# Performance work log

Measured on AMD Instinct MI355X. Metric: run time of the kernel, lower is better.

Reference implementation:

```python
import jax, jax.numpy as jnp
import numpy as np

SHAPES = np.array([[92, 92], [46, 46], [23, 23], [12, 12]], dtype=np.int32)
EMB, HID, H, L, P = 256, 256, 8, 4, 4


def setup_inputs() -> dict:
    key = jax.random.key(0)
    ks = jax.random.split(key, 10)
    I = int(SHAPES.prod(-1).sum())  # 11253 total pyramid pixels
    B, N = 2, I                      # dense encoder-style queries
    img = jax.random.normal(ks[0], (B, I, EMB), jnp.float32)
    queries = jax.random.normal(ks[1], (B, N, EMB), jnp.float32)
    reference_points = jax.random.uniform(ks[2], (B, N, 2), jnp.float32)
    s = 0.02  # keep offsets small so sampling points stay near [0,1]
    W_img = s * jax.random.normal(ks[3], (EMB, HID), jnp.float32)
    b_img = s * jax.random.normal(ks[4], (HID,), jnp.float32)
    W_q = s * jax.random.normal(ks[5], (EMB, H * L * P * 3), jnp.float32)
    b_q = s * jax.random.normal(ks[6], (H * L * P * 3,), jnp.float32)
    W_out = s * jax.random.normal(ks[7], (HID, EMB), jnp.float32)
    b_out = s * jax.random.normal(ks[8], (EMB,), jnp.float32)
    return dict(img=img, shapes=jnp.asarray(SHAPES), queries=queries,
                reference_points=reference_points, W_img=W_img, b_img=b_img,
                W_q=W_q, b_q=b_q, W_out=W_out, b_out=b_out)


def _msda(img_p, shapes_np, sp, aw):
    # img_p: [B,I,H,Cp], sp: [B,N,H,L,P,2] in [0,1] (x,y), aw: [B,N,H,L,P]
    B, I, Hh, Cp = img_p.shape
    N = sp.shape[1]
    imgT = img_p.transpose(0, 2, 1, 3)       # [B,H,I,Cp]
    awT = aw.transpose(0, 2, 1, 3, 4)        # [B,H,N,L,P]
    out = jnp.zeros((B, Hh, N, Cp), img_p.dtype)
    start = 0
    for l in range(shapes_np.shape[0]):
        h, w = int(shapes_np[l, 0]), int(shapes_np[l, 1])
        lvl = imgT[:, :, start:start + h * w]            # [B,H,h*w,Cp]
        start += h * w
        pts = sp[:, :, :, l].transpose(0, 2, 1, 3, 4)    # [B,H,N,P,2]
        # grid_sample(align_corners=True, border): pix = p*(size-1), clamped
        x = jnp.clip(pts[..., 0] * (w - 1), 0.0, w - 1)
        y = jnp.clip(pts[..., 1] * (h - 1), 0.0, h - 1)
        x0 = jnp.floor(x); y0 = jnp.floor(y)
        wx = x - x0; wy = y - y0
        x0i = x0.astype(jnp.int32); y0i = y0.astype(jnp.int32)
        x1i = jnp.minimum(x0i + 1, w - 1); y1i = jnp.minimum(y0i + 1, h - 1)

        def gat(yi, xi):
            idx = (yi * w + xi).reshape(B, Hh, N * P)
            g = jnp.take_along_axis(lvl, idx[..., None], axis=2)
            return g.reshape(B, Hh, N, P, Cp)

        v = (gat(y0i, x0i) * ((1 - wy) * (1 - wx))[..., None]
             + gat(y0i, x1i) * ((1 - wy) * wx)[..., None]
             + gat(y1i, x0i) * (wy * (1 - wx))[..., None]
             + gat(y1i, x1i) * (wy * wx)[..., None])     # [B,H,N,P,Cp]
        out = out + jnp.einsum('bhnpc,bhnp->bhnc', v, awT[:, :, :, l])
    return out.transpose(0, 2, 1, 3)                      # [B,N,H,Cp]


def reference(img, shapes, queries, reference_points, W_img, b_img, W_q, b_q, W_out, b_out):
    shapes_np = np.asarray(jax.device_get(shapes))
    B, I, C = img.shape
    N = queries.shape[1]
    Cp = HID // H
    img_p = (img @ W_img + b_img).reshape(B, I, H, Cp)
    qp = (queries @ W_q + b_q).reshape(B, N, H, L, P, 3)
    offsets = qp[..., :2]
    aw = jax.nn.softmax(qp[..., 2].reshape(B, N, H, L * P), axis=-1).reshape(B, N, H, L, P)
    sp = reference_points[:, :, None, None, None, :] + offsets  # [B,N,H,L,P,2]
    out = _msda(img_p, shapes_np, sp, aw)                        # [B,N,H,Cp]
    return out.reshape(B, N, HID) @ W_out + b_out
```

## Files before the change

kernel.cpp:

```cpp
#include <hip/hip_runtime.h>
#include <math.h>

#define NB    2
#define NQ    11253
#define NEMB  256
#define NHID  256
#define NH    8
#define NCP   32
#define MROWS (NB * NQ)
#define NGRP  (NB * NQ * NH)

__device__ __constant__ int LVL_H[4]     = {92, 46, 23, 12};
__device__ __constant__ int LVL_W[4]     = {92, 46, 23, 12};
__device__ __constant__ int LVL_START[4] = {0, 8464, 10580, 11109};

typedef float  f32x4  __attribute__((ext_vector_type(4)));
typedef __bf16 bf16x8 __attribute__((ext_vector_type(8)));
typedef short  s16x8  __attribute__((ext_vector_type(8)));

#define BM 128
#define BN 128
#define BK 32
#define LDK 40

__global__ __launch_bounds__(256) void gemm_mfma_split(
    const float* __restrict__ A, const float* __restrict__ B,
    const float* __restrict__ bias, float* __restrict__ C,
    int M, int N, int K)
{
    __shared__ __bf16 Ah[BM * LDK];
    __shared__ __bf16 Al[BM * LDK];
    __shared__ __bf16 Bh[BN * LDK];
    __shared__ __bf16 Bl[BN * LDK];

    const int t    = threadIdx.x;
    const int brow = blockIdx.x * BM;
    const int bcol = blockIdx.y * BN;
    const int wave = t >> 6;
    const int lane = t & 63;
    const int wr   = (wave >> 1) * 64;
    const int wc   = (wave & 1) * 64;
    const int l15  = lane & 15;
    const int l4   = lane >> 4;

    f32x4 acc[4][4] = {};

    const int ar = t >> 1;
    const int ak = (t & 1) * 16;
    const int bc2 = (t & 63) * 2;
    const int bk8 = (t >> 6) * 8;

    for (int k0 = 0; k0 < K; k0 += BK) {
        {
            float va[16];
            const int grow = brow + ar;
            if (grow < M) {
                const float* ap = A + (size_t)grow * K + k0 + ak;
                *(float4*)&va[0]  = *(const float4*)(ap + 0);
                *(float4*)&va[4]  = *(const float4*)(ap + 4);
                *(float4*)&va[8]  = *(const float4*)(ap + 8);
                *(float4*)&va[12] = *(const float4*)(ap + 12);
            } else {
                #pragma unroll
                for (int i = 0; i < 16; ++i) va[i] = 0.f;
            }
            bf16x8 h0, h1, l0, l1;
            #pragma unroll
            for (int i = 0; i < 8; ++i) {
                __bf16 h = (__bf16)va[i];
                h0[i] = h;  l0[i] = (__bf16)(va[i] - (float)h);
            }
            #pragma unroll
            for (int i = 0; i < 8; ++i) {
                __bf16 h = (__bf16)va[8 + i];
                h1[i] = h;  l1[i] = (__bf16)(va[8 + i] - (float)h);
            }
            *(bf16x8*)&Ah[ar * LDK + ak]     = h0;
            *(bf16x8*)&Ah[ar * LDK + ak + 8] = h1;
            *(bf16x8*)&Al[ar * LDK + ak]     = l0;
            *(bf16x8*)&Al[ar * LDK + ak + 8] = l1;
        }
        {
            bf16x8 h0, h1, l0, l1;
            #pragma unroll
            for (int j = 0; j < 8; ++j) {
                float2 v = *(const float2*)(B + (size_t)(k0 + bk8 + j) * N + bcol + bc2);
                __bf16 hx = (__bf16)v.x;
                __bf16 hy = (__bf16)v.y;
                h0[j] = hx;  l0[j] = (__bf16)(v.x - (float)hx);
                h1[j] = hy;  l1[j] = (__bf16)(v.y - (float)hy);
            }
            *(bf16x8*)&Bh[(bc2 + 0) * LDK + bk8] = h0;
            *(bf16x8*)&Bh[(bc2 + 1) * LDK + bk8] = h1;
            *(bf16x8*)&Bl[(bc2 + 0) * LDK + bk8] = l0;
            *(bf16x8*)&Bl[(bc2 + 1) * LDK + bk8] = l1;
        }
        __syncthreads();

        s16x8 a_h[4], a_l[4], b_h[4], b_l[4];
        #pragma unroll
        for (int mi = 0; mi < 4; ++mi) {
            int off = (wr + mi * 16 + l15) * LDK + l4 * 8;
            a_h[mi] = *(s16x8*)&Ah[off];
            a_l[mi] = *(s16x8*)&Al[off];
        }
        #pragma unroll
        for (int ni = 0; ni < 4; ++ni) {
            int off = (wc + ni * 16 + l15) * LDK + l4 * 8;
            b_h[ni] = *(s16x8*)&Bh[off];
            b_l[ni] = *(s16x8*)&Bl[off];
        }
        #pragma unroll
        for (int mi = 0; mi < 4; ++mi)
            #pragma unroll
            for (int ni = 0; ni < 4; ++ni) {
                acc[mi][ni] = __builtin_amdgcn_mfma_f32_16x16x32_bf16(a_h[mi], b_h[ni], acc[mi][ni], 0, 0, 0);
                acc[mi][ni] = __builtin_amdgcn_mfma_f32_16x16x32_bf16(a_h[mi], b_l[ni], acc[mi][ni], 0, 0, 0);
                acc[mi][ni] = __builtin_amdgcn_mfma_f32_16x16x32_bf16(a_l[mi], b_h[ni], acc[mi][ni], 0, 0, 0);
            }
        __syncthreads();
    }

    #pragma unroll
    for (int ni = 0; ni < 4; ++ni) {
        const int col = bcol + wc + ni * 16 + l15;
        const float bv = bias[col];
        #pragma unroll
        for (int mi = 0; mi < 4; ++mi) {
            #pragma unroll
            for (int j = 0; j < 4; ++j) {
                int row = brow + wr + mi * 16 + l4 * 4 + j;
                if (row < M) C[(size_t)row * N + col] = acc[mi][ni][j] + bv;
            }
        }
    }
}

__global__ __launch_bounds__(256) void msda_kernel(
    const float* __restrict__ img_p, const float* __restrict__ qp,
    const float* __restrict__ refp, float* __restrict__ out)
{
    __shared__ int smem[16][32][8];
    const int t  = threadIdx.x;
    const int t3 = t & 7;
    const int g  = t >> 3;
    int gid = blockIdx.x * 32 + g;
    const bool valid = gid < NGRP;
    if (!valid) gid = NGRP - 1;
    const int h  = gid & 7;
    const int bn = gid >> 3;
    const int b  = (bn >= NQ) ? 1 : 0;

    const float* q  = qp + (size_t)bn * 384 + h * 48;
    const float rx = refp[bn * 2 + 0];
    const float ry = refp[bn * 2 + 1];

    const float ox0 = q[t3 * 3 + 0],        oy0 = q[t3 * 3 + 1],        sc0 = q[t3 * 3 + 2];
    const float ox1 = q[(t3 + 8) * 3 + 0],  oy1 = q[(t3 + 8) * 3 + 1],  sc1 = q[(t3 + 8) * 3 + 2];

    float mx = fmaxf(sc0, sc1);
    mx = fmaxf(mx, __shfl_xor(mx, 1, 8));
    mx = fmaxf(mx, __shfl_xor(mx, 2, 8));
    mx = fmaxf(mx, __shfl_xor(mx, 4, 8));
    const float e0 = __expf(sc0 - mx);
    const float e1 = __expf(sc1 - mx);
    float sum = e0 + e1;
    sum += __shfl_xor(sum, 1, 8);
    sum += __shfl_xor(sum, 2, 8);
    sum += __shfl_xor(sum, 4, 8);
    const float inv = 1.0f / sum;

    #pragma unroll
    for (int which = 0; which < 2; ++which) {
        const int   s  = which ? (t3 + 8) : t3;
        const float ox = which ? ox1 : ox0;
        const float oy = which ? oy1 : oy0;
        const float aw = (which ? e1 : e0) * inv;
        const int l  = s >> 2;
        const int hh = LVL_H[l], ww = LVL_W[l], st = LVL_START[l];
        float x = (rx + ox) * (float)(ww - 1);
        float y = (ry + oy) * (float)(hh - 1);
        x = fminf(fmaxf(x, 0.f), (float)(ww - 1));
        y = fminf(fmaxf(y, 0.f), (float)(hh - 1));
        const float x0f = floorf(x), y0f = floorf(y);
        const int   x0 = (int)x0f,  y0 = (int)y0f;
        const float wx = x - x0f,   wy = y - y0f;
        const int dxb = (x0 < ww - 1) ? (NH * NCP * 4) : 0;
        const int dyb = (y0 < hh - 1) ? (ww * NH * NCP * 4) : 0;
        const int o00 = (st + y0 * ww + x0) * (NH * NCP * 4);
        const float u0 = aw * (1.f - wx), u1 = aw * wx;
        int4 pa = make_int4(o00, dxb, dyb, __float_as_int(u0 * (1.f - wy)));
        int4 pb = make_int4(__float_as_int(u1 * (1.f - wy)),
                            __float_as_int(u0 * wy),
                            __float_as_int(u1 * wy), 0);
        *(int4*)&smem[s][g][0] = pa;
        *(int4*)&smem[s][g][4] = pb;
    }
    __syncthreads();

    const char* base = (const char*)img_p
        + (((size_t)b * NQ * (NH * NCP) + h * NCP + t3 * 4) * 4);
    f32x4 acc = {0.f, 0.f, 0.f, 0.f};
    #pragma unroll
    for (int s = 0; s < 16; ++s) {
        const int4 pa = *(int4*)&smem[s][g][0];
        const int4 pb = *(int4*)&smem[s][g][4];
        const int o00 = pa.x;
        const int o01 = o00 + pa.y;
        const int o10 = o00 + pa.z;
        const int o11 = o10 + pa.y;
        const f32x4 v00 = *(const f32x4*)(base + o00);
        const f32x4 v01 = *(const f32x4*)(base + o01);
        const f32x4 v10 = *(const f32x4*)(base + o10);
        const f32x4 v11 = *(const f32x4*)(base + o11);
        acc += v00 * __int_as_float(pa.w);
        acc += v01 * __int_as_float(pb.x);
        acc += v10 * __int_as_float(pb.y);
        acc += v11 * __int_as_float(pb.z);
    }
    if (valid)
        *(f32x4*)(out + (size_t)bn * NHID + h * NCP + t3 * 4) = acc;
}

extern "C" void kernel_launch(void* const* d_in, const int* in_sizes, int n_in,
                              void* d_out, int out_size, void* d_ws, size_t ws_size,
                              hipStream_t stream) {
    const float* img     = (const float*)d_in[0];
    const float* queries = (const float*)d_in[2];
    const float* refp    = (const float*)d_in[3];
    const float* W_img   = (const float*)d_in[4];
    const float* b_img   = (const float*)d_in[5];
    const float* W_q     = (const float*)d_in[6];
    const float* b_q     = (const float*)d_in[7];
    const float* W_out   = (const float*)d_in[8];
    const float* b_out   = (const float*)d_in[9];
    float* out = (float*)d_out;

    float* ws = (float*)d_ws;
    float* img_p    = ws;
    float* qp       = img_p + (size_t)MROWS * NHID;
    float* msda_out = qp + (size_t)MROWS * 384;

    const int gRows = (MROWS + BM - 1) / BM;

    gemm_mfma_split<<<dim3(gRows, NHID / BN), 256, 0, stream>>>(
        img, W_img, b_img, img_p, MROWS, NHID, NEMB);
    gemm_mfma_split<<<dim3(gRows, 384 / BN), 256, 0, stream>>>(
        queries, W_q, b_q, qp, MROWS, 384, NEMB);
    msda_kernel<<<(NGRP + 31) / 32, 256, 0, stream>>>(img_p, qp, refp, msda_out);
    gemm_mfma_split<<<dim3(gRows, NEMB / BN), 256, 0, stream>>>(
        msda_out, W_out, b_out, out, MROWS, NEMB, NHID);
}
```

Before: 239.6 us.

## Pre-split GEMM operands into transposed bf16 hi/lo buffers before the GEMMs

Weights are converted once per call into transposed bf16 hi/lo pairs, so the GEMM B-tile loads become contiguous vector loads with no per-tile float-to-bf16 split. When the workspace is large enough, the img and query activations are also pre-split in separate conversion kernels. The MSDA kernel now writes its output directly as bf16 hi/lo for the final GEMM. This adds extra kernel launches and a full extra pass over the activations, trading redundant in-GEMM conversion work (repeated for every column block) against that added memory traffic.

```diff
diff --git a/kernel.cpp b/kernel.cpp
--- a/kernel.cpp
+++ b/kernel.cpp
@@ -16,15 +16,66 @@
 
 typedef float  f32x4  __attribute__((ext_vector_type(4)));
 typedef __bf16 bf16x8 __attribute__((ext_vector_type(8)));
+typedef __bf16 bf16x4v __attribute__((ext_vector_type(4)));
 typedef short  s16x8  __attribute__((ext_vector_type(8)));
+
+__global__ __launch_bounds__(256) void convert_hilo(
+    const float* __restrict__ src, __bf16* __restrict__ hi,
+    __bf16* __restrict__ lo, int nch)
+{
+    int i = blockIdx.x * 256 + threadIdx.x;
+    const int stride = gridDim.x * 256;
+    for (; i < nch; i += stride) {
+        const float* p = src + (size_t)i * 8;
+        float4 a = *(const float4*)p;
+        float4 b = *(const float4*)(p + 4);
+        float v[8] = {a.x, a.y, a.z, a.w, b.x, b.y, b.z, b.w};
+        bf16x8 h, l;
+        #pragma unroll
+        for (int j = 0; j < 8; ++j) {
+            __bf16 hh = (__bf16)v[j];
+            h[j] = hh; l[j] = (__bf16)(v[j] - (float)hh);
+        }
+        *(bf16x8*)(hi + (size_t)i * 8) = h;
+        *(bf16x8*)(lo + (size_t)i * 8) = l;
+    }
+}
+
+__global__ __launch_bounds__(256) void convert_w_T(
+    const float* __restrict__ W_img, const float* __restrict__ W_q,
+    const float* __restrict__ W_out,
+    __bf16* __restrict__ WiTh, __bf16* __restrict__ WiTl,
+    __bf16* __restrict__ WqTh, __bf16* __restrict__ WqTl,
+    __bf16* __restrict__ WoTh, __bf16* __restrict__ WoTl)
+{
+    int idx = blockIdx.x * 256 + threadIdx.x;
+    const float* W; __bf16 *Th, *Tl; int Nn, r;
+    if (idx < 8192)       { W = W_img; Th = WiTh; Tl = WiTl; Nn = 256; r = idx; }
+    else if (idx < 20480) { W = W_q;   Th = WqTh; Tl = WqTl; Nn = 384; r = idx - 8192; }
+    else                  { W = W_out; Th = WoTh; Tl = WoTl; Nn = 256; r = idx - 20480; }
+    const int n  = r % Nn;
+    const int k0 = (r / Nn) * 8;
+    bf16x8 h, l;
+    #pragma unroll
+    for (int j = 0; j < 8; ++j) {
+        float v = W[(size_t)(k0 + j) * Nn + n];
+        __bf16 hh = (__bf16)v;
+        h[j] = hh; l[j] = (__bf16)(v - (float)hh);
+    }
+    *(bf16x8*)(Th + (size_t)n * 256 + k0) = h;
+    *(bf16x8*)(Tl + (size_t)n * 256 + k0) = l;
+}
 
 #define BM 128
 #define BN 128
 #define BK 32
 #define LDK 40
 
-__global__ __launch_bounds__(256) void gemm_mfma_split(
-    const float* __restrict__ A, const float* __restrict__ B,
+template<bool PREA>
+__global__ __launch_bounds__(256) void gemm_mfma(
+    const float* __restrict__ A32,
+    const __bf16* __restrict__ Ah_g, const __bf16* __restrict__ Al_g,
+    const __bf16* __restrict__ BhT, const __bf16* __restrict__ BlT,
     const float* __restrict__ bias, float* __restrict__ C,
     int M, int N, int K)
 {
@@ -47,15 +98,26 @@
 
     const int ar = t >> 1;
     const int ak = (t & 1) * 16;
-    const int bc2 = (t & 63) * 2;
-    const int bk8 = (t >> 6) * 8;
+    const int grow = brow + ar;
+    const int bcr = t >> 1;
 
     for (int k0 = 0; k0 < K; k0 += BK) {
-        {
+        if constexpr (PREA) {
+            s16x8 h0 = {}, h1 = {}, l0 = {}, l1 = {};
+            if (grow < M) {
+                const __bf16* hp = Ah_g + (size_t)grow * K + k0 + ak;
+                const __bf16* lp = Al_g + (size_t)grow * K + k0 + ak;
+                h0 = *(const s16x8*)hp;  h1 = *(const s16x8*)(hp + 8);
+                l0 = *(const s16x8*)lp;  l1 = *(const s16x8*)(lp + 8);
+            }
+            *(s16x8*)&Ah[ar * LDK + ak]     = h0;
+            *(s16x8*)&Ah[ar * LDK + ak + 8] = h1;
+            *(s16x8*)&Al[ar * LDK + ak]     = l0;
+            *(s16x8*)&Al[ar * LDK + ak + 8] = l1;
+        } else {
             float va[16];
-            const int grow = brow + ar;
             if (grow < M) {
-                const float* ap = A + (size_t)grow * K + k0 + ak;
+                const float* ap = A32 + (size_t)grow * K + k0 + ak;
                 *(float4*)&va[0]  = *(const float4*)(ap + 0);
                 *(float4*)&va[4]  = *(const float4*)(ap + 4);
                 *(float4*)&va[8]  = *(const float4*)(ap + 8);
@@ -81,19 +143,14 @@
             *(bf16x8*)&Al[ar * LDK + ak + 8] = l1;
         }
         {
-            bf16x8 h0, h1, l0, l1;
-            #pragma unroll
-            for (int j = 0; j < 8; ++j) {
-                float2 v = *(const float2*)(B + (size_t)(k0 + bk8 + j) * N + bcol + bc2);
-                __bf16 hx = (__bf16)v.x;
-                __bf16 hy = (__bf16)v.y;
-                h0[j] = hx;  l0[j] = (__bf16)(v.x - (float)hx);
-                h1[j] = hy;  l1[j] = (__bf16)(v.y - (float)hy);
-            }
-            *(bf16x8*)&Bh[(bc2 + 0) * LDK + bk8] = h0;
-            *(bf16x8*)&Bh[(bc2 + 1) * LDK + bk8] = h1;
-            *(bf16x8*)&Bl[(bc2 + 0) * LDK + bk8] = l0;
-            *(bf16x8*)&Bl[(bc2 + 1) * LDK + bk8] = l1;
+            const __bf16* bp = BhT + (size_t)(bcol + bcr) * K + k0 + ak;
+            const __bf16* lp = BlT + (size_t)(bcol + bcr) * K + k0 + ak;
+            s16x8 h0 = *(const s16x8*)bp, h1 = *(const s16x8*)(bp + 8);
+            s16x8 l0 = *(const s16x8*)lp, l1 = *(const s16x8*)(lp + 8);
+            *(s16x8*)&Bh[bcr * LDK + ak]     = h0;
+            *(s16x8*)&Bh[bcr * LDK + ak + 8] = h1;
+            *(s16x8*)&Bl[bcr * LDK + ak]     = l0;
+            *(s16x8*)&Bl[bcr * LDK + ak + 8] = l1;
         }
         __syncthreads();
 
@@ -138,7 +195,8 @@
 
 __global__ __launch_bounds__(256) void msda_kernel(
     const float* __restrict__ img_p, const float* __restrict__ qp,
-    const float* __restrict__ refp, float* __restrict__ out)
+    const float* __restrict__ refp,
+    __bf16* __restrict__ outH, __bf16* __restrict__ outL)
 {
     __shared__ int smem[16][32][8];
     const int t  = threadIdx.x;
@@ -218,8 +276,17 @@
         acc += v10 * __int_as_float(pb.y);
         acc += v11 * __int_as_float(pb.z);
     }
-    if (valid)
-        *(f32x4*)(out + (size_t)bn * NHID + h * NCP + t3 * 4) = acc;
+    if (valid) {
+        bf16x4v hv, lv;
+        #pragma unroll
+        for (int j = 0; j < 4; ++j) {
+            __bf16 hh = (__bf16)acc[j];
+            hv[j] = hh; lv[j] = (__bf16)(acc[j] - (float)hh);
+        }
+        const size_t o = (size_t)bn * NHID + h * NCP + t3 * 4;
+        *(bf16x4v*)(outH + o) = hv;
+        *(bf16x4v*)(outL + o) = lv;
+    }
 }
 
 extern "C" void kernel_launch(void* const* d_in, const int* in_sizes, int n_in,
@@ -236,18 +303,46 @@
     const float* b_out   = (const float*)d_in[9];
     float* out = (float*)d_out;
 
-    float* ws = (float*)d_ws;
-    float* img_p    = ws;
-    float* qp       = img_p + (size_t)MROWS * NHID;
-    float* msda_out = qp + (size_t)MROWS * 384;
+    const size_t NA = (size_t)MROWS * 256;
+    float*  img_p = (float*)d_ws;
+    float*  qp    = img_p + NA;
+    __bf16* msdaH = (__bf16*)(qp + (size_t)MROWS * 384);
+    __bf16* msdaL = msdaH + NA;
+    __bf16* WiTh  = msdaL + NA;
+    __bf16* WiTl  = WiTh + 256 * 256;
+    __bf16* WqTh  = WiTl + 256 * 256;
+    __bf16* WqTl  = WqTh + 384 * 256;
+    __bf16* WoTh  = WqTl + 384 * 256;
+    __bf16* WoTl  = WoTh + 256 * 256;
+    __bf16* baseEnd = WoTl + 256 * 256;
+    __bf16* imgH = baseEnd;
+    __bf16* imgL = imgH + NA;
+    __bf16* qH   = imgL + NA;
+    __bf16* qL   = qH + NA;
+    const size_t need_full = (size_t)((char*)(qL + NA) - (char*)d_ws);
+    const bool FULL = ws_size >= need_full;
 
     const int gRows = (MROWS + BM - 1) / BM;
 
-    gemm_mfma_split<<<dim3(gRows, NHID / BN), 256, 0, stream>>>(
-        img, W_img, b_img, img_p, MROWS, NHID, NEMB);
-    gemm_mfma_split<<<dim3(gRows, 384 / BN), 256, 0, stream>>>(
-        queries, W_q, b_q, qp, MROWS, 384, NEMB);
-    msda_kernel<<<(NGRP + 31) / 32, 256, 0, stream>>>(img_p, qp, refp, msda_out);
-    gemm_mfma_split<<<dim3(gRows, NEMB / BN), 256, 0, stream>>>(
-        msda_out, W_out, b_out, out, MROWS, NEMB, NHID);
-}
+    convert_w_T<<<112, 256, 0, stream>>>(W_img, W_q, W_out,
+                                         WiTh, WiTl, WqTh, WqTl, WoTh, WoTl);
+
+    if (FULL) {
+        convert_hilo<<<2048, 256, 0, stream>>>(img,     imgH, imgL, (int)(NA / 8));
+        convert_hilo<<<2048, 256, 0, stream>>>(queries, qH,   qL,   (int)(NA / 8));
+        gemm_mfma<true><<<dim3(gRows, 2), 256, 0, stream>>>(
+            nullptr, imgH, imgL, WiTh, WiTl, b_img, img_p, MROWS, 256, 256);
+        gemm_mfma<true><<<dim3(gRows, 3), 256, 0, stream>>>(
+            nullptr, qH, qL, WqTh, WqTl, b_q, qp, MROWS, 384, 256);
+    } else {
+        gemm_mfma<false><<<dim3(gRows, 2), 256, 0, stream>>>(
+            img, nullptr, nullptr, WiTh, WiTl, b_img, img_p, MROWS, 256, 256);
+        gemm_mfma<false><<<dim3(gRows, 3), 256, 0, stream>>>(
+            queries, nullptr, nullptr, WqTh, WqTl, b_q, qp, MROWS, 384, 256);
+    }
+
+    msda_kernel<<<(NGRP + 31) / 32, 256, 0, stream>>>(img_p, qp, refp, msdaH, msdaL);
+
+    gemm_mfma<true><<<dim3(gRows, 2), 256, 0, stream>>>(
+        nullptr, msdaH, msdaL, WoTh, WoTl, b_out, out, MROWS, 256, 256);
+}
```

Measured after the change: 252.6 us. 1.05x slower.
